# Performance work log

Measured on AMD Instinct MI355X. Metric: run time of the kernel, lower is better.

Reference implementation:

```python
import jax, jax.numpy as jnp
import numpy as np

N, E, B, D, L, IN, H = 50000, 800000, 64, 64, 4, 7, 4


def _leaky(x, s=0.2):
    return jnp.where(x >= 0, x, s * x)


def _layernorm(x, g, b, eps=1e-5):
    mu = x.mean(-1, keepdims=True)
    v = ((x - mu) ** 2).mean(-1, keepdims=True)
    return (x - mu) * jax.lax.rsqrt(v + eps) * g + b


def _forward(x, edge_index, batch,
             enc_W, enc_b,
             gat_Wl, gat_Wr, gat_att, gat_b,
             ln_g, ln_b, ffn_W1, ffn_b1, ffn_W2, ffn_b2,
             n2g_W1, n2g_b1, n2g_W2, n2g_b2,
             g2n_W1, g2n_b1, g2n_W2, g2n_b2,
             dec_W1, dec_b1, dec_W2, dec_b2):
    n = x.shape[0]
    loops = jnp.arange(n, dtype=edge_index.dtype)
    src = jnp.concatenate([edge_index[0], loops])  # PyG add_self_loops=True
    dst = jnp.concatenate([edge_index[1], loops])

    h = x @ enc_W + enc_b  # encoder [N, D]
    for l in range(L):
        # ---- GATv2Conv(heads=4, concat=False), eval mode (dropout off) ----
        xl = (h @ gat_Wl[l]).reshape(n, H, D)  # source transform (lin_l)
        xr = (h @ gat_Wr[l]).reshape(n, H, D)  # target transform (lin_r)
        s = xl[src] + xr[dst]                              # [Et, H, D]
        e = jnp.sum(_leaky(s) * gat_att[l], axis=-1)       # [Et, H]
        m = jax.ops.segment_max(e, dst, num_segments=n)
        a = jnp.exp(e - m[dst])
        denom = jax.ops.segment_sum(a, dst, num_segments=n)
        a = a / (denom[dst] + 1e-16)                       # segment softmax
        out = jax.ops.segment_sum(a[..., None] * xl[src], dst, num_segments=n)
        out = out.mean(axis=1) + gat_b[l]                  # head average + bias
        # ---- residual + LayerNorm + FFN ----
        h2 = _layernorm(h + out, ln_g[l], ln_b[l])
        h = h2 + (_leaky(h2 @ ffn_W1[l] + ffn_b1[l]) @ ffn_W2[l] + ffn_b2[l])
        # ---- GlobalContextLayer ----
        lat = jax.nn.gelu(h @ n2g_W1[l] + n2g_b1[l]) @ n2g_W2[l] + n2g_b2[l]
        cnt = jax.ops.segment_sum(jnp.ones((n, 1), h.dtype), batch, num_segments=B)
        gmean = jax.ops.segment_sum(lat, batch, num_segments=B) / jnp.maximum(cnt, 1.0)
        gmax = jax.ops.segment_max(lat, batch, num_segments=B)
        gl = jnp.concatenate([gmean, gmax], axis=1)        # [B, 2D]
        ctx = jax.nn.gelu(gl @ g2n_W1[l] + g2n_b1[l]) @ g2n_W2[l] + g2n_b2[l]
        h = h + ctx[batch]
    return jax.nn.gelu(h @ dec_W1 + dec_b1) @ dec_W2 + dec_b2  # [N, 2]


def setup_inputs() -> dict:
    key = jax.random.key(0)
    ks = jax.random.split(key, 16)
    f = lambda i, s: jax.random.normal(ks[i], s, dtype=jnp.float32) * 0.1
    z = lambda s: jnp.zeros(s, jnp.float32)
    return dict(
        x=jax.random.normal(ks[0], (N, IN), dtype=jnp.float32),
        edge_index=jax.random.randint(ks[1], (2, E), 0, N, dtype=jnp.int32),
        batch=jnp.sort(jax.random.randint(ks[2], (N,), 0, B, dtype=jnp.int32)),
        enc_W=f(3, (IN, D)), enc_b=z((D,)),
        gat_Wl=f(4, (L, D, H * D)), gat_Wr=f(5, (L, D, H * D)),
        gat_att=f(6, (L, H, D)), gat_b=z((L, D)),
        ln_g=jnp.ones((L, D), jnp.float32), ln_b=z((L, D)),
        ffn_W1=f(7, (L, D, 2 * D)), ffn_b1=z((L, 2 * D)),
        ffn_W2=f(8, (L, 2 * D, D)), ffn_b2=z((L, D)),
        n2g_W1=f(9, (L, D, D)), n2g_b1=z((L, D)),
        n2g_W2=f(10, (L, D, D)), n2g_b2=z((L, D)),
        g2n_W1=f(11, (L, 2 * D, D)), g2n_b1=z((L, D)),
        g2n_W2=f(12, (L, D, D)), g2n_b2=z((L, D)),
        dec_W1=f(13, (D, D)), dec_b1=z((D,)),
        dec_W2=f(14, (D, 2)), dec_b2=z((2,)),
    )


def reference(x, edge_index, batch, enc_W, enc_b, gat_Wl, gat_Wr, gat_att, gat_b,
              ln_g, ln_b, ffn_W1, ffn_b1, ffn_W2, ffn_b2,
              n2g_W1, n2g_b1, n2g_W2, n2g_b2,
              g2n_W1, g2n_b1, g2n_W2, g2n_b2,
              dec_W1, dec_b1, dec_W2, dec_b2):
    return _forward(x, edge_index, batch, enc_W, enc_b, gat_Wl, gat_Wr, gat_att, gat_b,
                    ln_g, ln_b, ffn_W1, ffn_b1, ffn_W2, ffn_b2,
                    n2g_W1, n2g_b1, n2g_W2, n2g_b2,
                    g2n_W1, g2n_b1, g2n_W2, g2n_b2,
                    dec_W1, dec_b1, dec_W2, dec_b2)
```

## Files before the change

### kernel.cpp

```cpp
#include <hip/hip_runtime.h>
#include <hip/hip_bf16.h>
#include <math.h>

#define NN 50000
#define EE 800000
#define BBATCH 64
#define DDIM 64
#define NLAYER 4
#define NIN 7
#define NHEAD 4

typedef __attribute__((ext_vector_type(8))) short short8v;
typedef __attribute__((ext_vector_type(4))) float f32x4;

static __device__ __forceinline__ float wave_sum(float v) {
#pragma unroll
  for (int m = 32; m > 0; m >>= 1) v += __shfl_xor(v, m, 64);
  return v;
}

static __device__ __forceinline__ float gelu_t(float x) {
  float z = 0.7978845608f * (x + 0.044715f * x * x * x);
  float t = 2.f / (1.f + __expf(-2.f * z)) - 1.f;
  return 0.5f * x * (1.f + t);
}

static __device__ __forceinline__ unsigned short f2b(float v) {
  __hip_bfloat16 b = __float2bfloat16(v);
  return *reinterpret_cast<unsigned short*>(&b);
}

static __device__ __forceinline__ unsigned fkey(float x) {
  unsigned u = __builtin_bit_cast(unsigned, x);
  return (u >> 31) ? ~u : (u | 0x80000000u);
}
static __device__ __forceinline__ float fkey_inv(unsigned k) {
  unsigned u = (k & 0x80000000u) ? (k ^ 0x80000000u) : ~k;
  return __builtin_bit_cast(float, u);
}

template <int CTRL>
static __device__ __forceinline__ float dppf(float v) {
  int x = __builtin_amdgcn_mov_dpp(__builtin_bit_cast(int, v), CTRL, 0xF, 0xF, true);
  return __builtin_bit_cast(float, x);
}

static __device__ __forceinline__ void unpack8(uint4 u, float* xs) {
  unsigned int w[4] = {u.x, u.y, u.z, u.w};
#pragma unroll
  for (int k = 0; k < 4; k++) {
    xs[2 * k]     = __builtin_bit_cast(float, w[k] << 16);
    xs[2 * k + 1] = __builtin_bit_cast(float, w[k] & 0xFFFF0000u);
  }
}

static __device__ __forceinline__ short8v pack8(const float* v) {
  short8v r;
#pragma unroll
  for (int j = 0; j < 8; j++) r[j] = (short)f2b(v[j]);
  return r;
}

__global__ void k_count_edges(const int* __restrict__ dst, int e, int* cnt) {
  int i = blockIdx.x * blockDim.x + threadIdx.x;
  if (i < e) atomicAdd(&cnt[dst[i]], 1);
}

__global__ void k_scan_bsum(const int* __restrict__ cnt, int n, int* bsum) {
  __shared__ int red[256];
  int b = blockIdx.x, t = threadIdx.x;
  int s = 0;
  for (int i = b * 1024 + t; i < (b + 1) * 1024; i += 256)
    if (i < n) s += cnt[i] + 1;
  red[t] = s;
  __syncthreads();
  for (int o = 128; o > 0; o >>= 1) {
    if (t < o) red[t] += red[t + o];
    __syncthreads();
  }
  if (t == 0) bsum[b] = red[0];
}

__global__ void k_scan_offsets(int* bsum, int nb) {
  if (threadIdx.x == 0 && blockIdx.x == 0) {
    int acc = 0;
    for (int i = 0; i < nb; i++) { int v = bsum[i]; bsum[i] = acc; acc += v; }
  }
}

__global__ void k_scan_final(int* __restrict__ cnt, int n,
                             const int* __restrict__ bsum, int* __restrict__ indptr,
                             int* __restrict__ esrc) {
  __shared__ int lds[256];
  int b = blockIdx.x, t = threadIdx.x;
  int base = b * 1024;
  int v[4];
  int s = 0;
#pragma unroll
  for (int j = 0; j < 4; j++) {
    int i = base + t * 4 + j;
    v[j] = (i < n) ? cnt[i] + 1 : 0;
    s += v[j];
  }
  lds[t] = s;
  __syncthreads();
  for (int o = 1; o < 256; o <<= 1) {
    int x = (t >= o) ? lds[t - o] : 0;
    __syncthreads();
    lds[t] += x;
    __syncthreads();
  }
  int run = bsum[b] + lds[t] - s;
#pragma unroll
  for (int j = 0; j < 4; j++) {
    int i = base + t * 4 + j;
    if (i < n) {
      indptr[i] = run;
      esrc[run] = i;
      cnt[i] = run + 1;
    } else if (i == n) {
      indptr[n] = run;
    }
    run += v[j];
  }
}

__global__ void k_csr_fill(const int* __restrict__ src, const int* __restrict__ dst,
                           int e, int* nxt, int* esrc) {
  int i = blockIdx.x * blockDim.x + threadIdx.x;
  if (i < e) {
    int p = atomicAdd(&nxt[dst[i]], 1);
    esrc[p] = src[i];
  }
}

__global__ void k_batch_starts(const int* __restrict__ batch, int n, int nb, int* starts) {
  int i = blockIdx.x * blockDim.x + threadIdx.x;
  if (i >= n) return;
  int b = batch[i];
  if (i == 0) {
    for (int x = 0; x <= b; x++) starts[x] = 0;
  } else {
    int pb = batch[i - 1];
    if (pb != b)
      for (int x = pb + 1; x <= b; x++) starts[x] = i;
  }
  if (i == n - 1) {
    for (int x = b + 1; x <= nb; x++) starts[x] = n;
  }
}

#define SEG_LR (4 * 512 * 64)
#define SEG_F1 (4 * 128 * 64)
#define SEG_F2 (4 * 64 * 128)
#define SEG_N  (4 * 64 * 64)
#define SEG_D  (64 * 64)
#define WPREP_TOTAL (SEG_LR + SEG_F1 + SEG_F2 + 2 * SEG_N + SEG_D)
__global__ void k_wprep_all(const float* __restrict__ Wl, const float* __restrict__ Wr,
                            const float* __restrict__ F1, const float* __restrict__ F2,
                            const float* __restrict__ N1, const float* __restrict__ N2,
                            const float* __restrict__ D1,
                            unsigned short* __restrict__ wLR, unsigned short* __restrict__ wF1,
                            unsigned short* __restrict__ wF2, unsigned short* __restrict__ wN1,
                            unsigned short* __restrict__ wN2, unsigned short* __restrict__ wD1) {
  int idx = blockIdx.x * blockDim.x + threadIdx.x;
  if (idx < SEG_LR) {
    int l = idx / (512 * 64), rem = idx % (512 * 64);
    int c = rem / 64, k = rem % 64;
    float v = (c < 256) ? Wl[(size_t)l * 64 * 256 + k * 256 + c]
                        : Wr[(size_t)l * 64 * 256 + k * 256 + (c - 256)];
    wLR[idx] = f2b(v);
    return;
  }
  idx -= SEG_LR;
  if (idx < SEG_F1) {
    int l = idx / (128 * 64), rem = idx % (128 * 64);
    int c = rem / 64, k = rem % 64;
    wF1[idx] = f2b(F1[(size_t)l * 64 * 128 + k * 128 + c]);
    return;
  }
  idx -= SEG_F1;
  if (idx < SEG_F2) {
    int l = idx / (64 * 128), rem = idx % (64 * 128);
    int c = rem / 128, k = rem % 128;
    wF2[idx] = f2b(F2[(size_t)l * 128 * 64 + k * 64 + c]);
    return;
  }
  idx -= SEG_F2;
  if (idx < SEG_N) {
    int l = idx / (64 * 64), rem = idx % (64 * 64);
    int c = rem / 64, k = rem % 64;
    wN1[idx] = f2b(N1[(size_t)l * 64 * 64 + k * 64 + c]);
    return;
  }
  idx -= SEG_N;
  if (idx < SEG_N) {
    int l = idx / (64 * 64), rem = idx % (64 * 64);
    int c = rem / 64, k = rem % 64;
    wN2[idx] = f2b(N2[(size_t)l * 64 * 64 + k * 64 + c]);
    return;
  }
  idx -= SEG_N;
  if (idx < SEG_D) {
    int c = idx / 64, k = idx % 64;
    wD1[idx] = f2b(D1[k * 64 + c]);
  }
}

__global__ void k_encoder(const float* __restrict__ x, const float* __restrict__ W,
                          const float* __restrict__ bias, float* __restrict__ h, int n) {
  int idx = blockIdx.x * blockDim.x + threadIdx.x;
  if (idx >= n * 64) return;
  int i = idx >> 6, d = idx & 63;
  float acc = bias[d];
#pragma unroll
  for (int k = 0; k < NIN; k++) acc += x[i * NIN + k] * W[k * 64 + d];
  h[idx] = acc;
}

template <bool CTX>
__global__ __launch_bounds__(256) void k_xlr(const float* __restrict__ A,
                                             const float* __restrict__ ctxv,
                                             const int* __restrict__ batch,
                                             const unsigned short* __restrict__ Wt,
                                             unsigned short* __restrict__ Cb, int n) {
  const int lane = threadIdx.x & 63, wave = threadIdx.x >> 6;
  const int row0 = blockIdx.x * 64 + wave * 16;
  const int karow = (lane >> 4) * 8;
  const int arow0 = row0 + (lane & 15);
  const int arow = arow0 < n ? arow0 : 0;
  const float* ap = A + (size_t)arow * 64;

  float av[16];
  {
    float4 f0 = *(const float4*)(ap + karow);
    float4 f1 = *(const float4*)(ap + karow + 4);
    float4 f2 = *(const float4*)(ap + 32 + karow);
    float4 f3 = *(const float4*)(ap + 32 + karow + 4);
    av[0] = f0.x; av[1] = f0.y; av[2] = f0.z; av[3] = f0.w;
    av[4] = f1.x; av[5] = f1.y; av[6] = f1.z; av[7] = f1.w;
    av[8] = f2.x; av[9] = f2.y; av[10] = f2.z; av[11] = f2.w;
    av[12] = f3.x; av[13] = f3.y; av[14] = f3.z; av[15] = f3.w;
    if (CTX) {
      const float* cp = ctxv + batch[arow] * 64;
      float4 c0v = *(const float4*)(cp + karow);
      float4 c1v = *(const float4*)(cp + karow + 4);
      float4 c2v = *(const float4*)(cp + 32 + karow);
      float4 c3v = *(const float4*)(cp + 32 + karow + 4);
      av[0] += c0v.x; av[1] += c0v.y; av[2] += c0v.z; av[3] += c0v.w;
      av[4] += c1v.x; av[5] += c1v.y; av[6] += c1v.z; av[7] += c1v.w;
      av[8] += c2v.x; av[9] += c2v.y; av[10] += c2v.z; av[11] += c2v.w;
      av[12] += c3v.x; av[13] += c3v.y; av[14] += c3v.z; av[15] += c3v.w;
    }
  }
  short8v a0 = pack8(av), a1 = pack8(av + 8);

#pragma unroll
  for (int cb = 0; cb < 8; cb++) {
#pragma unroll
    for (int cc = 0; cc < 4; cc++) {
      const int c = cb * 64 + cc * 16 + (lane & 15);
      f32x4 t = {0.f, 0.f, 0.f, 0.f};
      t = __builtin_amdgcn_mfma_f32_16x16x32_bf16(a0, *(const short8v*)(Wt + (size_t)c * 64 + karow), t, 0, 0, 0);
      t = __builtin_amdgcn_mfma_f32_16x16x32_bf16(a1, *(const short8v*)(Wt + (size_t)c * 64 + 32 + karow), t, 0, 0, 0);
#pragma unroll
      for (int r = 0; r < 4; r++) {
        const int row = row0 + (lane >> 4) * 4 + r;
        if (row < n) Cb[(size_t)row * 512 + c] = f2b(t[r]);
      }
    }
  }
}

__global__ __launch_bounds__(256) void k_fnp(const unsigned short* __restrict__ A,
                                             const unsigned short* __restrict__ F1t,
                                             const float* __restrict__ fb1,
                                             const unsigned short* __restrict__ F2t,
                                             const float* __restrict__ fb2,
                                             const float* __restrict__ res,
                                             float* __restrict__ hOut,
                                             const unsigned short* __restrict__ N1t,
                                             const float* __restrict__ nb1,
                                             const unsigned short* __restrict__ N2t,
                                             const float* __restrict__ nb2,
                                             const int* __restrict__ batch,
                                             float* __restrict__ psum,
                                             unsigned int* __restrict__ pmax, int n) {
  __shared__ unsigned short tl[4][16 * 136];
  __shared__ unsigned short tn[4][16 * 72];
  __shared__ float s_sum[64];
  __shared__ unsigned s_max[64];
  const int lane = threadIdx.x & 63, wave = threadIdx.x >> 6;
  const int row0b = blockIdx.x * 64;
  const int row0 = row0b + wave * 16;
  const int karow = (lane >> 4) * 8;
  const int arow = row0 + (lane & 15);
  const size_t abase = (size_t)(arow < n ? arow : 0) * 64 + karow;
  if (threadIdx.x < 64) { s_sum[threadIdx.x] = 0.f; s_max[threadIdx.x] = 0u; }
  short8v a0 = *(const short8v*)(A + abase);
  short8v a1 = *(const short8v*)(A + abase + 32);

#pragma unroll
  for (int cc = 0; cc < 8; cc++) {
    const int c = cc * 16 + (lane & 15);
    f32x4 t = {0.f, 0.f, 0.f, 0.f};
    t = __builtin_amdgcn_mfma_f32_16x16x32_bf16(a0, *(const short8v*)(F1t + (size_t)c * 64 + karow), t, 0, 0, 0);
    t = __builtin_amdgcn_mfma_f32_16x16x32_bf16(a1, *(const short8v*)(F1t + (size_t)c * 64 + 32 + karow), t, 0, 0, 0);
    const float bv = fb1[c];
#pragma unroll
    for (int r = 0; r < 4; r++) {
      float v = t[r] + bv;
      v = fmaxf(v, 0.2f * v);
      int rr = (lane >> 4) * 4 + r;
      tl[wave][rr * 136 + c] = f2b(v);
    }
  }

  short8v a2[4];
#pragma unroll
  for (int f = 0; f < 4; f++)
    a2[f] = *(const short8v*)(&tl[wave][(lane & 15) * 136 + f * 32 + karow]);

#pragma unroll
  for (int cc = 0; cc < 4; cc++) {
    const int c = cc * 16 + (lane & 15);
    f32x4 t = {0.f, 0.f, 0.f, 0.f};
#pragma unroll
    for (int f = 0; f < 4; f++)
      t = __builtin_amdgcn_mfma_f32_16x16x32_bf16(a2[f], *(const short8v*)(F2t + (size_t)c * 128 + f * 32 + karow), t, 0, 0, 0);
    const float bv = fb2[c];
#pragma unroll
    for (int r = 0; r < 4; r++) {
      const int row = row0 + (lane >> 4) * 4 + r;
      const int rr = (lane >> 4) * 4 + r;
      float v = t[r] + bv + ((row < n) ? res[(size_t)row * 64 + c] : 0.f);
      if (row < n) hOut[(size_t)row * 64 + c] = v;
      tn[wave][rr * 72 + c] = f2b(v);
    }
  }

  short8v a3[2];
#pragma unroll
  for (int f = 0; f < 2; f++)
    a3[f] = *(const short8v*)(&tn[wave][(lane & 15) * 72 + f * 32 + karow]);

#pragma unroll
  for (int cc = 0; cc < 4; cc++) {
    const int c = cc * 16 + (lane & 15);
    f32x4 t = {0.f, 0.f, 0.f, 0.f};
    t = __builtin_amdgcn_mfma_f32_16x16x32_bf16(a3[0], *(const short8v*)(N1t + (size_t)c * 64 + karow), t, 0, 0, 0);
    t = __builtin_amdgcn_mfma_f32_16x16x32_bf16(a3[1], *(const short8v*)(N1t + (size_t)c * 64 + 32 + karow), t, 0, 0, 0);
    const float bv = nb1[c];
#pragma unroll
    for (int r = 0; r < 4; r++) {
      int rr = (lane >> 4) * 4 + r;
      tl[wave][rr * 72 + c] = f2b(gelu_t(t[r] + bv));
    }
  }

  short8v a4[2];
#pragma unroll
  for (int f = 0; f < 2; f++)
    a4[f] = *(const short8v*)(&tl[wave][(lane & 15) * 72 + f * 32 + karow]);

  float pv[4][4];
#pragma unroll
  for (int cc = 0; cc < 4; cc++) {
    const int c = cc * 16 + (lane & 15);
    f32x4 t = {0.f, 0.f, 0.f, 0.f};
    t = __builtin_amdgcn_mfma_f32_16x16x32_bf16(a4[0], *(const short8v*)(N2t + (size_t)c * 64 + karow), t, 0, 0, 0);
    t = __builtin_amdgcn_mfma_f32_16x16x32_bf16(a4[1], *(const short8v*)(N2t + (size_t)c * 64 + 32 + karow), t, 0, 0, 0);
    const float bv = nb2[c];
#pragma unroll
    for (int r = 0; r < 4; r++) pv[cc][r] = t[r] + bv;
  }

  __syncthreads();
  const int blo = batch[row0b];
  const int last = row0b + 63 < n ? row0b + 63 : n - 1;
  const int bhi = batch[last];
  if (blo == bhi && row0b + 63 < n) {
#pragma unroll
    for (int cc = 0; cc < 4; cc++) {
      const int c = cc * 16 + (lane & 15);
      float s = pv[cc][0] + pv[cc][1] + pv[cc][2] + pv[cc][3];
      float mx = fmaxf(fmaxf(pv[cc][0], pv[cc][1]), fmaxf(pv[cc][2], pv[cc][3]));
      atomicAdd(&s_sum[c], s);
      atomicMax(&s_max[c], fkey(mx));
    }
    __syncthreads();
    if (threadIdx.x < 64) {
      atomicAdd(&psum[blo * 64 + threadIdx.x], s_sum[threadIdx.x]);
      atomicMax(&pmax[blo * 64 + threadIdx.x], s_max[threadIdx.x]);
    }
  } else {
#pragma unroll
    for (int cc = 0; cc < 4; cc++) {
      const int c = cc * 16 + (lane & 15);
#pragma unroll
      for (int r = 0; r < 4; r++) {
        const int row = row0 + (lane >> 4) * 4 + r;
        if (row < n) {
          const int b = batch[row];
          atomicAdd(&psum[b * 64 + c], pv[cc][r]);
          atomicMax(&pmax[b * 64 + c], fkey(pv[cc][r]));
        }
      }
    }
  }
}

template <bool CTX>
__global__ __launch_bounds__(256) void k_gat(const unsigned short* __restrict__ xlr,
                                             const float* __restrict__ att,
                                             const float* __restrict__ gbias,
                                             const float* __restrict__ lng,
                                             const float* __restrict__ lnb,
                                             const float* __restrict__ h,
                                             const float* __restrict__ ctxv,
                                             const int* __restrict__ batch,
                                             const int* __restrict__ indptr,
                                             const int* __restrict__ esrc,
                                             float* __restrict__ h2,
                                             unsigned short* __restrict__ h2b, int n) {
  const int wave = threadIdx.x >> 6, lane = threadIdx.x & 63;
  const int node = blockIdx.x * 4 + wave;
  if (node >= n) return;
  const int q = lane >> 4, r = lane & 15;
  const int c = r & 3;
  const int doff = (r >> 2) * 64 + c * 16;

  float xr_d[16], att_d[16];
  {
    const uint4* xp = (const uint4*)(xlr + (size_t)node * 512 + 256 + doff);
    uint4 u0 = xp[0], u1 = xp[1];
    unpack8(u0, xr_d);
    unpack8(u1, xr_d + 8);
    const float4* ap = (const float4*)(att + doff);
#pragma unroll
    for (int k = 0; k < 4; k++) {
      float4 a = ap[k];
      att_d[4 * k] = a.x; att_d[4 * k + 1] = a.y;
      att_d[4 * k + 2] = a.z; att_d[4 * k + 3] = a.w;
    }
  }

  float acc[16] = {};
  float den = 0.f;
  const int beg = indptr[node], end = indptr[node + 1];

  int j0 = beg + q;
  int s_cur = esrc[(j0 < end) ? j0 : beg];
  const uint4* xp0 = (const uint4*)(xlr + (size_t)s_cur * 512 + doff);
  uint4 u0 = xp0[0], u1 = xp0[1];
  int jn1 = beg + 4 + q;
  int s_nxt = esrc[(jn1 < end && beg + 4 < end) ? jn1 : beg];

  for (int jb = beg; jb < end; jb += 4) {
    const uint4 cu0 = u0, cu1 = u1;
    const bool cvalid = (jb + q) < end;
    if (jb + 4 < end) {
      const uint4* xpn = (const uint4*)(xlr + (size_t)s_nxt * 512 + doff);
      u0 = xpn[0];
      u1 = xpn[1];
      if (jb + 8 < end) {
        const int jn = jb + 8 + q;
        s_nxt = esrc[(jn < end) ? jn : beg];
      }
    }
    float xs[16];
    unpack8(cu0, xs);
    unpack8(cu1, xs + 8);
    float p0 = 0.f, p1 = 0.f, p2 = 0.f, p3 = 0.f;
#pragma unroll
    for (int k = 0; k < 4; k++) {
      float t0 = xs[4 * k + 0] + xr_d[4 * k + 0]; t0 = fmaxf(t0, 0.2f * t0); p0 = fmaf(t0, att_d[4 * k + 0], p0);
      float t1 = xs[4 * k + 1] + xr_d[4 * k + 1]; t1 = fmaxf(t1, 0.2f * t1); p1 = fmaf(t1, att_d[4 * k + 1], p1);
      float t2 = xs[4 * k + 2] + xr_d[4 * k + 2]; t2 = fmaxf(t2, 0.2f * t2); p2 = fmaf(t2, att_d[4 * k + 2], p2);
      float t3 = xs[4 * k + 3] + xr_d[4 * k + 3]; t3 = fmaxf(t3, 0.2f * t3); p3 = fmaf(t3, att_d[4 * k + 3], p3);
    }
    float p = (p0 + p1) + (p2 + p3);
    p += dppf<0xB1>(p);
    p += dppf<0x4E>(p);
    const float pw = cvalid ? __expf(fminf(p, 60.f)) : 0.f;
    den += pw;
#pragma unroll
    for (int d = 0; d < 16; d++) acc[d] = fmaf(pw, xs[d], acc[d]);
  }

  den += __shfl_xor(den, 16, 64);
  den += __shfl_xor(den, 32, 64);
#pragma unroll
  for (int d = 0; d < 16; d++) {
    acc[d] += __shfl_xor(acc[d], 16, 64);
    acc[d] += __shfl_xor(acc[d], 32, 64);
  }

  const float rden = 0.25f / (den + 1e-16f);
  float y[16];
  float s4 = 0.f;
  const float4* hp = (const float4*)(h + (size_t)node * 64 + c * 16);
  const float4* gp = (const float4*)(gbias + c * 16);
  const float4* cp = CTX ? (const float4*)(ctxv + batch[node] * 64 + c * 16) : nullptr;
#pragma unroll
  for (int k = 0; k < 4; k++) {
    float4 hv = hp[k], gv = gp[k];
    if (CTX) {
      float4 cv = cp[k];
      hv.x += cv.x; hv.y += cv.y; hv.z += cv.z; hv.w += cv.w;
    }
    float hf[4] = {hv.x, hv.y, hv.z, hv.w};
    float gf[4] = {gv.x, gv.y, gv.z, gv.w};
#pragma unroll
    for (int d2 = 0; d2 < 4; d2++) {
      int d = 4 * k + d2;
      float v = acc[d] * rden;
      v += dppf<0x124>(v);
      v += dppf<0x128>(v);
      y[d] = hf[d2] + v + gf[d2];
      s4 += y[d];
    }
  }

  const float mu = wave_sum(s4) * (1.f / 1024.f);
  float v4 = 0.f;
  float dv[16];
#pragma unroll
  for (int d = 0; d < 16; d++) {
    dv[d] = y[d] - mu;
    v4 += dv[d] * dv[d];
  }
  const float var = wave_sum(v4) * (1.f / 1024.f);
  const float rstd = rsqrtf(var + 1e-5f);

  if (lane < 4) {
    float4* outp = (float4*)(h2 + (size_t)node * 64 + lane * 16);
    uint2* outb = (uint2*)(h2b + (size_t)node * 64 + lane * 16);
    const float4* lgp = (const float4*)(lng + lane * 16);
    const float4* lbp = (const float4*)(lnb + lane * 16);
#pragma unroll
    for (int k = 0; k < 4; k++) {
      float4 g = lgp[k], b = lbp[k];
      float o0 = dv[4 * k + 0] * rstd * g.x + b.x;
      float o1 = dv[4 * k + 1] * rstd * g.y + b.y;
      float o2 = dv[4 * k + 2] * rstd * g.z + b.z;
      float o3 = dv[4 * k + 3] * rstd * g.w + b.w;
      float4 of; of.x = o0; of.y = o1; of.z = o2; of.w = o3;
      outp[k] = of;
      uint2 pk;
      pk.x = (unsigned int)f2b(o0) | ((unsigned int)f2b(o1) << 16);
      pk.y = (unsigned int)f2b(o2) | ((unsigned int)f2b(o3) << 16);
      outb[k] = pk;
    }
  }
}

__global__ void k_ctx2(const float* __restrict__ psum, const unsigned int* __restrict__ pmax,
                       const int* __restrict__ starts,
                       const float* __restrict__ W1, const float* __restrict__ b1,
                       const float* __restrict__ W2, const float* __restrict__ b2,
                       float* __restrict__ ctx) {
  int b = blockIdx.x;
  int t = threadIdx.x;
  __shared__ float g[128], tt[64];
  int cnt = starts[b + 1] - starts[b];
  if (t < 64) {
    g[t] = psum[b * 64 + t] / fmaxf((float)cnt, 1.0f);
  } else {
    g[t] = fkey_inv(pmax[b * 64 + (t - 64)]);
  }
  __syncthreads();
  if (t < 64) {
    float acc = b1[t];
    for (int k = 0; k < 128; k++) acc += g[k] * W1[k * 64 + t];
    tt[t] = gelu_t(acc);
  }
  __syncthreads();
  if (t < 64) {
    float acc2 = b2[t];
    for (int k = 0; k < 64; k++) acc2 += tt[k] * W2[k * 64 + t];
    ctx[b * 64 + t] = acc2;
  }
}

__global__ __launch_bounds__(256) void k_dec(const float* __restrict__ A,
                                             const float* __restrict__ ctxv,
                                             const int* __restrict__ batch,
                                             const unsigned short* __restrict__ W1t,
                                             const float* __restrict__ b1,
                                             const float* __restrict__ W2,
                                             const float* __restrict__ b2,
                                             float* __restrict__ out, int n) {
  const int lane = threadIdx.x & 63, wave = threadIdx.x >> 6;
  const int row0 = blockIdx.x * 64 + wave * 16;
  const int karow = (lane >> 4) * 8;
  const int arow0 = row0 + (lane & 15);
  const int arow = arow0 < n ? arow0 : 0;
  const float* ap = A + (size_t)arow * 64;
  const float* cp = ctxv + batch[arow] * 64;

  float av[16];
  {
    float4 f0 = *(const float4*)(ap + karow);
    float4 f1 = *(const float4*)(ap + karow + 4);
    float4 f2 = *(const float4*)(ap + 32 + karow);
    float4 f3 = *(const float4*)(ap + 32 + karow + 4);
    float4 c0v = *(const float4*)(cp + karow);
    float4 c1v = *(const float4*)(cp + karow + 4);
    float4 c2v = *(const float4*)(cp + 32 + karow);
    float4 c3v = *(const float4*)(cp + 32 + karow + 4);
    av[0] = f0.x + c0v.x; av[1] = f0.y + c0v.y; av[2] = f0.z + c0v.z; av[3] = f0.w + c0v.w;
    av[4] = f1.x + c1v.x; av[5] = f1.y + c1v.y; av[6] = f1.z + c1v.z; av[7] = f1.w + c1v.w;
    av[8] = f2.x + c2v.x; av[9] = f2.y + c2v.y; av[10] = f2.z + c2v.z; av[11] = f2.w + c2v.w;
    av[12] = f3.x + c3v.x; av[13] = f3.y + c3v.y; av[14] = f3.z + c3v.z; av[15] = f3.w + c3v.w;
  }
  short8v a0 = pack8(av), a1 = pack8(av + 8);

  float o0[4] = {}, o1[4] = {};
#pragma unroll
  for (int cc = 0; cc < 4; cc++) {
    const int cidx = cc * 16 + (lane & 15);
    f32x4 t = {0.f, 0.f, 0.f, 0.f};
    t = __builtin_amdgcn_mfma_f32_16x16x32_bf16(a0, *(const short8v*)(W1t + (size_t)cidx * 64 + karow), t, 0, 0, 0);
    t = __builtin_amdgcn_mfma_f32_16x16x32_bf16(a1, *(const short8v*)(W1t + (size_t)cidx * 64 + 32 + karow), t, 0, 0, 0);
    const float bv = b1[cidx];
    const float w0 = W2[cidx * 2 + 0], w1 = W2[cidx * 2 + 1];
#pragma unroll
    for (int r = 0; r < 4; r++) {
      float v = gelu_t(t[r] + bv);
      o0[r] = fmaf(v, w0, o0[r]);
      o1[r] = fmaf(v, w1, o1[r]);
    }
  }
#pragma unroll
  for (int m = 1; m < 16; m <<= 1) {
#pragma unroll
    for (int r = 0; r < 4; r++) {
      o0[r] += __shfl_xor(o0[r], m, 64);
      o1[r] += __shfl_xor(o1[r], m, 64);
    }
  }
  if ((lane & 15) == 0) {
#pragma unroll
    for (int r = 0; r < 4; r++) {
      const int row = row0 + (lane >> 4) * 4 + r;
      if (row < n) {
        out[2 * row] = o0[r] + b2[0];
        out[2 * row + 1] = o1[r] + b2[1];
      }
    }
  }
}

extern "C" void kernel_launch(void* const* d_in, const int* in_sizes, int n_in,
                              void* d_out, int out_size, void* d_ws, size_t ws_size,
                              hipStream_t stream) {
  const float* x = (const float*)d_in[0];
  const int* ei = (const int*)d_in[1];
  const int* batch = (const int*)d_in[2];
  const float* enc_W = (const float*)d_in[3];
  const float* enc_b = (const float*)d_in[4];
  const float* gat_Wl = (const float*)d_in[5];
  const float* gat_Wr = (const float*)d_in[6];
  const float* gat_att = (const float*)d_in[7];
  const float* gat_b = (const float*)d_in[8];
  const float* ln_g = (const float*)d_in[9];
  const float* ln_b = (const float*)d_in[10];
  const float* ffn_W1 = (const float*)d_in[11];
  const float* ffn_b1 = (const float*)d_in[12];
  const float* ffn_W2 = (const float*)d_in[13];
  const float* ffn_b2 = (const float*)d_in[14];
  const float* n2g_W1 = (const float*)d_in[15];
  const float* n2g_b1 = (const float*)d_in[16];
  const float* n2g_W2 = (const float*)d_in[17];
  const float* n2g_b2 = (const float*)d_in[18];
  const float* g2n_W1 = (const float*)d_in[19];
  const float* g2n_b1 = (const float*)d_in[20];
  const float* g2n_W2 = (const float*)d_in[21];
  const float* g2n_b2 = (const float*)d_in[22];
  const float* dec_W1 = (const float*)d_in[23];
  const float* dec_b1 = (const float*)d_in[24];
  const float* dec_W2 = (const float*)d_in[25];
  const float* dec_b2 = (const float*)d_in[26];

  const int N = NN, E = EE;
  const int* e_src = ei;
  const int* e_dst = ei + E;

  float* h = (float*)d_ws;
  float* h2 = h + (size_t)N * 64;
  float* ctx = h2 + (size_t)N * 64;
  float* psum_all = ctx + BBATCH * 64;
  unsigned int* pmax_all = (unsigned int*)(psum_all + 4 * BBATCH * 64);
  int* cnt = (int*)(pmax_all + 4 * BBATCH * 64);
  int* indptr = cnt + N;
  int* esrc = indptr + N + 1;
  int* bsum = esrc + (E + N);
  int* starts = bsum + 64;
  size_t off = (size_t)(starts + BBATCH + 1) - (size_t)d_ws;
  off = (off + 15) & ~(size_t)15;
  unsigned short* h2b = (unsigned short*)((char*)d_ws + off);
  unsigned short* xlr = h2b + (size_t)N * 64;
  unsigned short* wLR = xlr + (size_t)N * 512;
  unsigned short* wF1 = wLR + SEG_LR;
  unsigned short* wF2 = wF1 + SEG_F1;
  unsigned short* wN1 = wF2 + SEG_F2;
  unsigned short* wN2 = wN1 + SEG_N;
  unsigned short* wD1 = wN2 + SEG_N;

  const int TPB = 256;
  const int NBLK_SCAN = (N + 1 + 1023) / 1024;

  hipMemsetAsync(psum_all, 0,
                 (size_t)4 * BBATCH * 64 * (sizeof(float) + sizeof(unsigned int)) + (size_t)N * sizeof(int),
                 stream);

  hipLaunchKernelGGL(k_wprep_all, dim3((WPREP_TOTAL + 255) / 256), dim3(256), 0, stream,
                     gat_Wl, gat_Wr, ffn_W1, ffn_W2, n2g_W1, n2g_W2, dec_W1,
                     wLR, wF1, wF2, wN1, wN2, wD1);

  hipLaunchKernelGGL(k_count_edges, dim3((E + TPB - 1) / TPB), dim3(TPB), 0, stream, e_dst, E, cnt);
  hipLaunchKernelGGL(k_scan_bsum, dim3(NBLK_SCAN), dim3(256), 0, stream, cnt, N, bsum);
  hipLaunchKernelGGL(k_scan_offsets, dim3(1), dim3(64), 0, stream, bsum, NBLK_SCAN);
  hipLaunchKernelGGL(k_scan_final, dim3(NBLK_SCAN), dim3(256), 0, stream, cnt, N, bsum, indptr, esrc);
  hipLaunchKernelGGL(k_csr_fill, dim3((E + TPB - 1) / TPB), dim3(TPB), 0, stream, e_src, e_dst, E, cnt, esrc);
  hipLaunchKernelGGL(k_batch_starts, dim3((N + TPB - 1) / TPB), dim3(TPB), 0, stream, batch, N, BBATCH, starts);

  hipLaunchKernelGGL(k_encoder, dim3((N * 64 + TPB - 1) / TPB), dim3(TPB), 0, stream,
                     x, enc_W, enc_b, h, N);

  const int GN = (N + 63) / 64;

  for (int l = 0; l < NLAYER; l++) {
    const unsigned short* LRt = wLR + (size_t)l * 512 * 64;
    const unsigned short* F1t = wF1 + (size_t)l * 128 * 64;
    const unsigned short* F2t = wF2 + (size_t)l * 64 * 128;
    const unsigned short* N1t = wN1 + (size_t)l * 64 * 64;
    const unsigned short* N2t = wN2 + (size_t)l * 64 * 64;
    const float* attl = gat_att + (size_t)l * 256;
    const float* gbl = gat_b + (size_t)l * 64;
    const float* lngl = ln_g + (size_t)l * 64;
    const float* lnbl = ln_b + (size_t)l * 64;
    const float* fb1 = ffn_b1 + (size_t)l * 128;
    const float* fb2 = ffn_b2 + (size_t)l * 64;
    const float* nb1 = n2g_b1 + (size_t)l * 64;
    const float* nb2 = n2g_b2 + (size_t)l * 64;
    const float* gW1 = g2n_W1 + (size_t)l * 128 * 64;
    const float* gb1 = g2n_b1 + (size_t)l * 64;
    const float* gW2 = g2n_W2 + (size_t)l * 64 * 64;
    const float* gb2 = g2n_b2 + (size_t)l * 64;
    float* psumL = psum_all + (size_t)l * BBATCH * 64;
    unsigned int* pmaxL = pmax_all + (size_t)l * BBATCH * 64;

    if (l == 0)
      hipLaunchKernelGGL((k_xlr<false>), dim3(GN), dim3(256), 0, stream,
                         h, nullptr, nullptr, LRt, xlr, N);
    else
      hipLaunchKernelGGL((k_xlr<true>), dim3(GN), dim3(256), 0, stream,
                         h, ctx, batch, LRt, xlr, N);
    if (l == 0)
      hipLaunchKernelGGL((k_gat<false>), dim3((N + 3) / 4), dim3(256), 0, stream,
                         xlr, attl, gbl, lngl, lnbl, h, nullptr, nullptr, indptr, esrc, h2, h2b, N);
    else
      hipLaunchKernelGGL((k_gat<true>), dim3((N + 3) / 4), dim3(256), 0, stream,
                         xlr, attl, gbl, lngl, lnbl, h, ctx, batch, indptr, esrc, h2, h2b, N);
    hipLaunchKernelGGL(k_fnp, dim3(GN), dim3(256), 0, stream,
                       h2b, F1t, fb1, F2t, fb2, h2, h,
                       N1t, nb1, N2t, nb2, batch, psumL, pmaxL, N);
    hipLaunchKernelGGL(k_ctx2, dim3(BBATCH), dim3(128), 0, stream,
                       psumL, pmaxL, starts, gW1, gb1, gW2, gb2, ctx);
  }

  hipLaunchKernelGGL(k_dec, dim3(GN), dim3(256), 0, stream,
                     h, ctx, batch, wD1, dec_b1, dec_W2, dec_b2, (float*)d_out, N);
}
```

Measured before the change: 836.1 us.

## Fuse context MLP into FFN kernel via last-block pattern; drop fp32 h2

Removes the separate k_ctx2 launch. The last block of k_fnp to finish, found through an atomic done counter, now computes the per-graph context MLP. It also stops writing the fp32 LayerNorm output h2 from the GAT kernel and reads the residual back from the bf16 copy instead. This saves a launch and N*64 fp32 of stores and loads per layer, but the residual now carries bf16 precision and the context MLP runs serially in a single block.

```diff
diff --git a/kernel.cpp b/kernel.cpp
--- a/kernel.cpp
+++ b/kernel.cpp
@@ -28,6 +28,10 @@
 static __device__ __forceinline__ unsigned short f2b(float v) {
   __hip_bfloat16 b = __float2bfloat16(v);
   return *reinterpret_cast<unsigned short*>(&b);
+}
+
+static __device__ __forceinline__ float b2f(unsigned short u) {
+  return __builtin_bit_cast(float, (unsigned int)u << 16);
 }
 
 static __device__ __forceinline__ unsigned fkey(float x) {
@@ -277,7 +281,6 @@
                                              const float* __restrict__ fb1,
                                              const unsigned short* __restrict__ F2t,
                                              const float* __restrict__ fb2,
-                                             const float* __restrict__ res,
                                              float* __restrict__ hOut,
                                              const unsigned short* __restrict__ N1t,
                                              const float* __restrict__ nb1,
@@ -285,7 +288,14 @@
                                              const float* __restrict__ nb2,
                                              const int* __restrict__ batch,
                                              float* __restrict__ psum,
-                                             unsigned int* __restrict__ pmax, int n) {
+                                             unsigned int* __restrict__ pmax,
+                                             const float* __restrict__ gW1,
+                                             const float* __restrict__ gb1,
+                                             const float* __restrict__ gW2,
+                                             const float* __restrict__ gb2,
+                                             const int* __restrict__ starts,
+                                             int* __restrict__ done,
+                                             float* __restrict__ ctxOut, int n) {
   __shared__ unsigned short tl[4][16 * 136];
   __shared__ unsigned short tn[4][16 * 72];
   __shared__ float s_sum[64];
@@ -333,7 +343,7 @@
     for (int r = 0; r < 4; r++) {
       const int row = row0 + (lane >> 4) * 4 + r;
       const int rr = (lane >> 4) * 4 + r;
-      float v = t[r] + bv + ((row < n) ? res[(size_t)row * 64 + c] : 0.f);
+      float v = t[r] + bv + ((row < n) ? b2f(A[(size_t)row * 64 + c]) : 0.f);
       if (row < n) hOut[(size_t)row * 64 + c] = v;
       tn[wave][rr * 72 + c] = f2b(v);
     }
@@ -407,6 +417,32 @@
         }
       }
     }
+  }
+
+  __threadfence();
+  __shared__ int lastFlag;
+  if (threadIdx.x == 0) lastFlag = (atomicAdd(done, 1) == (int)gridDim.x - 1);
+  __syncthreads();
+  if (!lastFlag) return;
+  __threadfence();
+
+  __shared__ float gg[4][128];
+  __shared__ float ttw[4][64];
+  for (int bb0 = 0; bb0 < BBATCH; bb0 += 4) {
+    const int bb = bb0 + wave;
+    float gm = atomicAdd(&psum[bb * 64 + lane], 0.0f);
+    unsigned km = atomicMax(&pmax[bb * 64 + lane], 0u);
+    const int cntb = starts[bb + 1] - starts[bb];
+    gg[wave][lane] = gm / fmaxf((float)cntb, 1.0f);
+    gg[wave][64 + lane] = fkey_inv(km);
+    __syncthreads();
+    float acc = gb1[lane];
+    for (int k = 0; k < 128; k++) acc += gg[wave][k] * gW1[k * 64 + lane];
+    ttw[wave][lane] = gelu_t(acc);
+    __syncthreads();
+    float acc2 = gb2[lane];
+    for (int k = 0; k < 64; k++) acc2 += ttw[wave][k] * gW2[k * 64 + lane];
+    ctxOut[bb * 64 + lane] = acc2;
   }
 }
 
@@ -421,7 +457,6 @@
                                              const int* __restrict__ batch,
                                              const int* __restrict__ indptr,
                                              const int* __restrict__ esrc,
-                                             float* __restrict__ h2,
                                              unsigned short* __restrict__ h2b, int n) {
   const int wave = threadIdx.x >> 6, lane = threadIdx.x & 63;
   const int node = blockIdx.x * 4 + wave;
@@ -534,7 +569,6 @@
   const float rstd = rsqrtf(var + 1e-5f);
 
   if (lane < 4) {
-    float4* outp = (float4*)(h2 + (size_t)node * 64 + lane * 16);
     uint2* outb = (uint2*)(h2b + (size_t)node * 64 + lane * 16);
     const float4* lgp = (const float4*)(lng + lane * 16);
     const float4* lbp = (const float4*)(lnb + lane * 16);
@@ -545,41 +579,11 @@
       float o1 = dv[4 * k + 1] * rstd * g.y + b.y;
       float o2 = dv[4 * k + 2] * rstd * g.z + b.z;
       float o3 = dv[4 * k + 3] * rstd * g.w + b.w;
-      float4 of; of.x = o0; of.y = o1; of.z = o2; of.w = o3;
-      outp[k] = of;
       uint2 pk;
       pk.x = (unsigned int)f2b(o0) | ((unsigned int)f2b(o1) << 16);
       pk.y = (unsigned int)f2b(o2) | ((unsigned int)f2b(o3) << 16);
       outb[k] = pk;
     }
-  }
-}
-
-__global__ void k_ctx2(const float* __restrict__ psum, const unsigned int* __restrict__ pmax,
-                       const int* __restrict__ starts,
-                       const float* __restrict__ W1, const float* __restrict__ b1,
-                       const float* __restrict__ W2, const float* __restrict__ b2,
-                       float* __restrict__ ctx) {
-  int b = blockIdx.x;
-  int t = threadIdx.x;
-  __shared__ float g[128], tt[64];
-  int cnt = starts[b + 1] - starts[b];
-  if (t < 64) {
-    g[t] = psum[b * 64 + t] / fmaxf((float)cnt, 1.0f);
-  } else {
-    g[t] = fkey_inv(pmax[b * 64 + (t - 64)]);
-  }
-  __syncthreads();
-  if (t < 64) {
-    float acc = b1[t];
-    for (int k = 0; k < 128; k++) acc += g[k] * W1[k * 64 + t];
-    tt[t] = gelu_t(acc);
-  }
-  __syncthreads();
-  if (t < 64) {
-    float acc2 = b2[t];
-    for (int k = 0; k < 64; k++) acc2 += tt[k] * W2[k * 64 + t];
-    ctx[b * 64 + t] = acc2;
   }
 }
 
@@ -688,11 +692,11 @@
   const int* e_dst = ei + E;
 
   float* h = (float*)d_ws;
-  float* h2 = h + (size_t)N * 64;
-  float* ctx = h2 + (size_t)N * 64;
+  float* ctx = h + (size_t)N * 64;
   float* psum_all = ctx + BBATCH * 64;
   unsigned int* pmax_all = (unsigned int*)(psum_all + 4 * BBATCH * 64);
-  int* cnt = (int*)(pmax_all + 4 * BBATCH * 64);
+  int* done = (int*)(pmax_all + 4 * BBATCH * 64);
+  int* cnt = done + 4;
   int* indptr = cnt + N;
   int* esrc = indptr + N + 1;
   int* bsum = esrc + (E + N);
@@ -712,7 +716,8 @@
   const int NBLK_SCAN = (N + 1 + 1023) / 1024;
 
   hipMemsetAsync(psum_all, 0,
-                 (size_t)4 * BBATCH * 64 * (sizeof(float) + sizeof(unsigned int)) + (size_t)N * sizeof(int),
+                 (size_t)4 * BBATCH * 64 * (sizeof(float) + sizeof(unsigned int)) +
+                 4 * sizeof(int) + (size_t)N * sizeof(int),
                  stream);
 
   hipLaunchKernelGGL(k_wprep_all, dim3((WPREP_TOTAL + 255) / 256), dim3(256), 0, stream,
@@ -760,15 +765,14 @@
                          h, ctx, batch, LRt, xlr, N);
     if (l == 0)
       hipLaunchKernelGGL((k_gat<false>), dim3((N + 3) / 4), dim3(256), 0, stream,
-                         xlr, attl, gbl, lngl, lnbl, h, nullptr, nullptr, indptr, esrc, h2, h2b, N);
+                         xlr, attl, gbl, lngl, lnbl, h, nullptr, nullptr, indptr, esrc, h2b, N);
     else
       hipLaunchKernelGGL((k_gat<true>), dim3((N + 3) / 4), dim3(256), 0, stream,
-                         xlr, attl, gbl, lngl, lnbl, h, ctx, batch, indptr, esrc, h2, h2b, N);
+                         xlr, attl, gbl, lngl, lnbl, h, ctx, batch, indptr, esrc, h2b, N);
     hipLaunchKernelGGL(k_fnp, dim3(GN), dim3(256), 0, stream,
-                       h2b, F1t, fb1, F2t, fb2, h2, h,
-                       N1t, nb1, N2t, nb2, batch, psumL, pmaxL, N);
-    hipLaunchKernelGGL(k_ctx2, dim3(BBATCH), dim3(128), 0, stream,
-                       psumL, pmaxL, starts, gW1, gb1, gW2, gb2, ctx);
+                       h2b, F1t, fb1, F2t, fb2, h,
+                       N1t, nb1, N2t, nb2, batch, psumL, pmaxL,
+                       gW1, gb1, gW2, gb2, starts, done + l, ctx, N);
   }
 
   hipLaunchKernelGGL(k_dec, dim3(GN), dim3(256), 0, stream,
```

After: 1.095 ms. 1.31x slower.
